# Performance work log

Hardware: AMD Instinct MI355X
Metric: run time of the kernel (lower is better)

## Reference

```python
import jax, jax.numpy as jnp
import numpy as np

POINT_SIZE = 1000000
LOC_DIM = 16
TIM_DIM = 16
POS_DIM = 32
INPUT_DIM = 5
HID = 32
EPS = 1e-5


def _linear(x, W, b):
    return x @ W.T + b


def _resnet(x, W1, b1, W2, b2):
    # Sequential(ReLU, Linear, ReLU, Linear, Dropout(eval=identity)); out = x + 0.3*net(x)
    h = jax.nn.relu(x)
    h = _linear(h, W1, b1)
    h = jax.nn.relu(h)
    h = _linear(h, W2, b2)
    return x + 0.3 * h


def _chain(x, rW1, rb1, rW2, rb2, W, b):
    for i in range(2):  # two ResNet blocks (fixed, structural)
        x = _resnet(x, rW1[i], rb1[i], rW2[i], rb2[i])
    return _linear(x, W, b)


def _mk_linear(key, out_dim, in_dim):
    k1, k2 = jax.random.split(key)
    s = 1.0 / np.sqrt(in_dim)
    W = jax.random.uniform(k1, (out_dim, in_dim), jnp.float32, -s, s)
    b = jax.random.uniform(k2, (out_dim,), jnp.float32, -s, s)
    return W, b


def _mk_res_stack(key, dim, n=2):
    ks = jax.random.split(key, 4 * n)
    W1s, b1s, W2s, b2s = [], [], [], []
    for i in range(n):
        W1, b1 = _mk_linear(ks[4 * i], dim, dim)
        W2, b2 = _mk_linear(ks[4 * i + 1], dim, dim)
        W1s.append(W1); b1s.append(b1); W2s.append(W2); b2s.append(b2)
    return jnp.stack(W1s), jnp.stack(b1s), jnp.stack(W2s), jnp.stack(b2s)


def setup_inputs() -> dict:
    key = jax.random.key(0)
    ks = iter(jax.random.split(key, 40))
    d = {}
    d["x"] = jax.random.randint(next(ks), (3,), 0, 24, dtype=jnp.int64 if jax.config.jax_enable_x64 else jnp.int32)
    d["hidden"] = jnp.zeros((1, 1, HID), jnp.float32)
    d["pos"] = 3
    # embeddings
    d["loc_emb"] = jax.random.normal(next(ks), (POINT_SIZE, LOC_DIM), jnp.float32)
    d["arr_emb"] = jax.random.normal(next(ks), (24, TIM_DIM), jnp.float32)
    d["dur_emb"] = jax.random.normal(next(ks), (24, TIM_DIM), jnp.float32)
    d["pos_emb"] = jax.random.normal(next(ks), (10, POS_DIM), jnp.float32)
    for name, dim in (("fc1", LOC_DIM), ("fc2", TIM_DIM), ("fc3", TIM_DIM)):
        rW1, rb1, rW2, rb2 = _mk_res_stack(next(ks), dim)
        W, b = _mk_linear(next(ks), INPUT_DIM, dim)
        d[f"{name}_rW1"], d[f"{name}_rb1"], d[f"{name}_rW2"], d[f"{name}_rb2"] = rW1, rb1, rW2, rb2
        d[f"{name}_W"], d[f"{name}_b"] = W, b
    # LayerNorm(15)
    d["ln_g"] = jnp.ones((3 * INPUT_DIM,), jnp.float32)
    d["ln_b"] = jnp.zeros((3 * INPUT_DIM,), jnp.float32)
    # ODE: Linear(5->32) + ResNet(32)
    d["ode_W"], d["ode_b"] = _mk_linear(next(ks), HID, INPUT_DIM)
    oW1, ob1, oW2, ob2 = _mk_res_stack(next(ks), HID, n=1)
    d["ode_rW1"], d["ode_rb1"], d["ode_rW2"], d["ode_rb2"] = oW1[0], ob1[0], oW2[0], ob2[0]
    # heads
    d["fc4_W"], d["fc4_b"] = _mk_linear(next(ks), POINT_SIZE, HID)
    d["fc5_W"], d["fc5_b"] = _mk_linear(next(ks), 24, HID)
    d["fc6_W"], d["fc6_b"] = _mk_linear(next(ks), 24, HID)
    # GRU (input 15, hidden 32)
    d["gru_Wih"], d["gru_bih"] = _mk_linear(next(ks), 3 * HID, 3 * INPUT_DIM)
    d["gru_Whh"], d["gru_bhh"] = _mk_linear(next(ks), 3 * HID, HID)
    return d


def reference(x, hidden, pos, loc_emb, arr_emb, dur_emb, pos_emb,
              fc1_rW1, fc1_rb1, fc1_rW2, fc1_rb2, fc1_W, fc1_b,
              fc2_rW1, fc2_rb1, fc2_rW2, fc2_rb2, fc2_W, fc2_b,
              fc3_rW1, fc3_rb1, fc3_rW2, fc3_rb2, fc3_W, fc3_b,
              ln_g, ln_b, ode_W, ode_b, ode_rW1, ode_rb1, ode_rW2, ode_rb2,
              fc4_W, fc4_b, fc5_W, fc5_b, fc6_W, fc6_b,
              gru_Wih, gru_bih, gru_Whh, gru_bhh):
    pos_e = pos_emb[pos]                                   # (32,)
    loc = _chain(loc_emb[x[0]], fc1_rW1, fc1_rb1, fc1_rW2, fc1_rb2, fc1_W, fc1_b)  # (5,)
    arr = _chain(arr_emb[x[1]], fc2_rW1, fc2_rb1, fc2_rW2, fc2_rb2, fc2_W, fc2_b)  # (5,)
    dur = _chain(dur_emb[x[2]], fc3_rW1, fc3_rb1, fc3_rW2, fc3_rb2, fc3_W, fc3_b)  # (5,)
    point = jnp.concatenate([loc, arr, dur])               # (15,)
    mu = jnp.mean(point)
    var = jnp.mean((point - mu) ** 2)
    point = (point - mu) * jax.lax.rsqrt(var + EPS) * ln_g + ln_b
    # hidden = hidden + ODE(dur)
    ode = _linear(dur, ode_W, ode_b)
    ode = _resnet(ode, ode_rW1, ode_rb1, ode_rW2, ode_rb2)
    h = hidden.reshape(-1) + ode                           # (32,)
    # single GRU step
    gi = gru_Wih @ point + gru_bih
    gh = gru_Whh @ h + gru_bhh
    i_r, i_z, i_n = jnp.split(gi, 3)
    h_r, h_z, h_n = jnp.split(gh, 3)
    r = jax.nn.sigmoid(i_r + h_r)
    z = jax.nn.sigmoid(i_z + h_z)
    n = jnp.tanh(i_n + r * h_n)
    h_new = (1.0 - z) * n + z * h                          # (32,) == out == new hidden
    next_loc = jax.nn.log_softmax(h_new @ fc4_W.T + fc4_b)
    next_arr = jax.nn.log_softmax((h_new + pos_e) @ fc5_W.T + fc5_b)
    next_dur = jax.nn.log_softmax(h_new @ fc6_W.T + fc6_b)
    return (next_loc, next_arr, next_dur, h_new.reshape(1, 1, HID))
```

## Files before the change

kernel.cpp:

```cpp
#include <hip/hip_runtime.h>
#include <math.h>

#define ROWS 1000000
#define K2_BLOCKS 1024
#define K2_THREADS 256

__global__ __launch_bounds__(128) void front_kernel(
    const int* __restrict__ x, const float* __restrict__ hidden, const int* __restrict__ pos,
    const float* __restrict__ loc_emb, const float* __restrict__ arr_emb,
    const float* __restrict__ dur_emb, const float* __restrict__ pos_emb,
    const float* __restrict__ f1rW1, const float* __restrict__ f1rb1,
    const float* __restrict__ f1rW2, const float* __restrict__ f1rb2,
    const float* __restrict__ f1W,   const float* __restrict__ f1b,
    const float* __restrict__ f2rW1, const float* __restrict__ f2rb1,
    const float* __restrict__ f2rW2, const float* __restrict__ f2rb2,
    const float* __restrict__ f2W,   const float* __restrict__ f2b,
    const float* __restrict__ f3rW1, const float* __restrict__ f3rb1,
    const float* __restrict__ f3rW2, const float* __restrict__ f3rb2,
    const float* __restrict__ f3W,   const float* __restrict__ f3b,
    const float* __restrict__ ln_g,  const float* __restrict__ ln_b,
    const float* __restrict__ ode_W, const float* __restrict__ ode_b,
    const float* __restrict__ oW1,   const float* __restrict__ ob1,
    const float* __restrict__ oW2,   const float* __restrict__ ob2,
    const float* __restrict__ fc5_W, const float* __restrict__ fc5_b,
    const float* __restrict__ fc6_W, const float* __restrict__ fc6_b,
    const float* __restrict__ gWih,  const float* __restrict__ gbih,
    const float* __restrict__ gWhh,  const float* __restrict__ gbhh,
    float* __restrict__ out, float* __restrict__ ws)
{
    __shared__ float e[3][16];
    __shared__ float tr[3][16];
    __shared__ float h1[3][16];
    __shared__ float praw[15];
    __shared__ float pnorm[15];
    __shared__ float ode0[32], odt[32], hvec[32], hnew[32], pe[32];
    __shared__ float gi[96], gh[96];
    __shared__ float a5[24], a6[24];
    __shared__ float red[4];

    const int t = threadIdx.x;

    if (t < 48) {
        int c = t >> 4, j = t & 15;
        const float* emb = (c == 0) ? (loc_emb + (size_t)x[0] * 16)
                         : (c == 1) ? (arr_emb + (size_t)x[1] * 16)
                                    : (dur_emb + (size_t)x[2] * 16);
        e[c][j] = emb[j];
    }
    if (t < 32) pe[t] = pos_emb[pos[0] * 32 + t];
    __syncthreads();

    for (int i = 0; i < 2; ++i) {
        if (t < 48) { int c = t >> 4, j = t & 15; tr[c][j] = fmaxf(e[c][j], 0.f); }
        __syncthreads();
        if (t < 48) {
            int c = t >> 4, j = t & 15;
            const float* W1 = ((c == 0) ? f1rW1 : (c == 1) ? f2rW1 : f3rW1) + i * 256 + j * 16;
            const float* b1 = ((c == 0) ? f1rb1 : (c == 1) ? f2rb1 : f3rb1) + i * 16;
            float a = b1[j];
            #pragma unroll
            for (int k = 0; k < 16; ++k) a += W1[k] * tr[c][k];
            h1[c][j] = fmaxf(a, 0.f);
        }
        __syncthreads();
        if (t < 48) {
            int c = t >> 4, j = t & 15;
            const float* W2 = ((c == 0) ? f1rW2 : (c == 1) ? f2rW2 : f3rW2) + i * 256 + j * 16;
            const float* b2 = ((c == 0) ? f1rb2 : (c == 1) ? f2rb2 : f3rb2) + i * 16;
            float a = b2[j];
            #pragma unroll
            for (int k = 0; k < 16; ++k) a += W2[k] * h1[c][k];
            e[c][j] += 0.3f * a;
        }
        __syncthreads();
    }

    if (t < 15) {
        int c = t / 5, q = t % 5;
        const float* W = ((c == 0) ? f1W : (c == 1) ? f2W : f3W) + q * 16;
        const float* b = ((c == 0) ? f1b : (c == 1) ? f2b : f3b);
        float a = b[q];
        #pragma unroll
        for (int k = 0; k < 16; ++k) a += W[k] * e[c][k];
        praw[t] = a;
    }
    __syncthreads();

    if (t == 0) {
        float mu = 0.f;
        for (int k = 0; k < 15; ++k) mu += praw[k];
        mu *= (1.f / 15.f);
        float var = 0.f;
        for (int k = 0; k < 15; ++k) { float d = praw[k] - mu; var += d * d; }
        var *= (1.f / 15.f);
        red[0] = mu;
        red[1] = rsqrtf(var + 1e-5f);
    }
    __syncthreads();
    if (t < 15) pnorm[t] = (praw[t] - red[0]) * red[1] * ln_g[t] + ln_b[t];

    if (t < 32) {
        float a = ode_b[t];
        const float* W = ode_W + t * 5;
        #pragma unroll
        for (int k = 0; k < 5; ++k) a += W[k] * praw[10 + k];
        ode0[t] = a;
    }
    __syncthreads();
    if (t < 32) {
        float a = ob1[t];
        const float* W = oW1 + t * 32;
        #pragma unroll
        for (int k = 0; k < 32; ++k) a += W[k] * fmaxf(ode0[k], 0.f);
        odt[t] = fmaxf(a, 0.f);
    }
    __syncthreads();
    if (t < 32) {
        float a = ob2[t];
        const float* W = oW2 + t * 32;
        #pragma unroll
        for (int k = 0; k < 32; ++k) a += W[k] * odt[k];
        hvec[t] = hidden[t] + ode0[t] + 0.3f * a;
    }
    __syncthreads();

    if (t < 96) {
        float a = gbih[t];
        const float* W = gWih + t * 15;
        #pragma unroll
        for (int k = 0; k < 15; ++k) a += W[k] * pnorm[k];
        gi[t] = a;
        float c2 = gbhh[t];
        const float* V = gWhh + t * 32;
        #pragma unroll
        for (int k = 0; k < 32; ++k) c2 += V[k] * hvec[k];
        gh[t] = c2;
    }
    __syncthreads();
    if (t < 32) {
        float r = 1.f / (1.f + expf(-(gi[t] + gh[t])));
        float z = 1.f / (1.f + expf(-(gi[32 + t] + gh[32 + t])));
        float n = tanhf(gi[64 + t] + r * gh[64 + t]);
        float hn = (1.f - z) * n + z * hvec[t];
        hnew[t] = hn;
        ws[t] = hn;
        out[ROWS + 48 + t] = hn;
    }
    __syncthreads();

    if (t < 24) {
        float a = fc5_b[t];
        const float* W = fc5_W + t * 32;
        #pragma unroll
        for (int k = 0; k < 32; ++k) a += W[k] * (hnew[k] + pe[k]);
        a5[t] = a;
        float b = fc6_b[t];
        const float* V = fc6_W + t * 32;
        #pragma unroll
        for (int k = 0; k < 32; ++k) b += V[k] * hnew[k];
        a6[t] = b;
    }
    __syncthreads();
    if (t == 0) {
        float m = -INFINITY;
        for (int k = 0; k < 24; ++k) m = fmaxf(m, a5[k]);
        float s = 0.f;
        for (int k = 0; k < 24; ++k) s += expf(a5[k] - m);
        red[2] = m + logf(s);
        m = -INFINITY;
        for (int k = 0; k < 24; ++k) m = fmaxf(m, a6[k]);
        s = 0.f;
        for (int k = 0; k < 24; ++k) s += expf(a6[k] - m);
        red[3] = m + logf(s);
    }
    __syncthreads();
    if (t < 24) {
        out[ROWS + t]      = a5[t] - red[2];
        out[ROWS + 24 + t] = a6[t] - red[3];
    }
}

__global__ __launch_bounds__(K2_THREADS) void logits_kernel(
    const float* __restrict__ W, const float* __restrict__ b,
    const float* __restrict__ ws_h, float* __restrict__ out,
    float* __restrict__ partials)
{
    __shared__ float hs[32];
    if (threadIdx.x < 32) hs[threadIdx.x] = ws_h[threadIdx.x];
    __syncthreads();

    float hr[32];
    #pragma unroll
    for (int k = 0; k < 32; ++k) hr[k] = hs[k];

    const float4* W4 = (const float4*)W;
    float m = -INFINITY, s = 0.f;

    for (int r = blockIdx.x * K2_THREADS + threadIdx.x; r < ROWS;
         r += K2_BLOCKS * K2_THREADS) {
        float acc = b[r];
        #pragma unroll
        for (int j = 0; j < 8; ++j) {
            float4 w = W4[(size_t)r * 8 + j];
            acc += w.x * hr[4 * j] + w.y * hr[4 * j + 1]
                 + w.z * hr[4 * j + 2] + w.w * hr[4 * j + 3];
        }
        out[r] = acc;
        if (acc > m) { s = s * expf(m - acc) + 1.f; m = acc; }
        else         { s += expf(acc - m); }
    }

    __shared__ float sm[K2_THREADS], ss[K2_THREADS];
    sm[threadIdx.x] = m; ss[threadIdx.x] = s;
    __syncthreads();
    for (int off = K2_THREADS / 2; off > 0; off >>= 1) {
        if (threadIdx.x < off) {
            float m2 = sm[threadIdx.x + off], s2 = ss[threadIdx.x + off];
            float M  = fmaxf(sm[threadIdx.x], m2);
            ss[threadIdx.x] = ss[threadIdx.x] * expf(sm[threadIdx.x] - M)
                            + s2 * expf(m2 - M);
            sm[threadIdx.x] = M;
        }
        __syncthreads();
    }
    if (threadIdx.x == 0) {
        partials[2 * blockIdx.x]     = sm[0];
        partials[2 * blockIdx.x + 1] = ss[0];
    }
}

__global__ __launch_bounds__(256) void lse_reduce_kernel(
    const float* __restrict__ partials, float* __restrict__ lse)
{
    __shared__ float sm[256], ss[256];
    const int t = threadIdx.x;
    float m = -INFINITY, s = 0.f;
    for (int i = t; i < K2_BLOCKS; i += 256) {
        float m2 = partials[2 * i], s2 = partials[2 * i + 1];
        float M = fmaxf(m, m2);
        s = s * ((m == -INFINITY) ? 0.f : expf(m - M)) + s2 * expf(m2 - M);
        m = M;
    }
    sm[t] = m; ss[t] = s;
    __syncthreads();
    for (int off = 128; off > 0; off >>= 1) {
        if (t < off) {
            float m2 = sm[t + off], s2 = ss[t + off];
            float M = fmaxf(sm[t], m2);
            ss[t] = ss[t] * expf(sm[t] - M) + s2 * expf(m2 - M);
            sm[t] = M;
        }
        __syncthreads();
    }
    if (t == 0) lse[0] = sm[0] + logf(ss[0]);
}

__global__ __launch_bounds__(256) void finalize_kernel(
    float* __restrict__ out, const float* __restrict__ lse)
{
    const int r4 = blockIdx.x * 256 + threadIdx.x;
    if (r4 < ROWS / 4) {
        const float l = lse[0];
        float4* o4 = (float4*)out;
        float4 v = o4[r4];
        v.x -= l; v.y -= l; v.z -= l; v.w -= l;
        o4[r4] = v;
    }
}

extern "C" void kernel_launch(void* const* d_in, const int* in_sizes, int n_in,
                              void* d_out, int out_size, void* d_ws, size_t ws_size,
                              hipStream_t stream) {
    const int*   x       = (const int*)  d_in[0];
    const float* hidden  = (const float*)d_in[1];
    const int*   pos     = (const int*)  d_in[2];
    const float* loc_emb = (const float*)d_in[3];
    const float* arr_emb = (const float*)d_in[4];
    const float* dur_emb = (const float*)d_in[5];
    const float* pos_emb = (const float*)d_in[6];
    const float* f1rW1 = (const float*)d_in[7];
    const float* f1rb1 = (const float*)d_in[8];
    const float* f1rW2 = (const float*)d_in[9];
    const float* f1rb2 = (const float*)d_in[10];
    const float* f1W   = (const float*)d_in[11];
    const float* f1b   = (const float*)d_in[12];
    const float* f2rW1 = (const float*)d_in[13];
    const float* f2rb1 = (const float*)d_in[14];
    const float* f2rW2 = (const float*)d_in[15];
    const float* f2rb2 = (const float*)d_in[16];
    const float* f2W   = (const float*)d_in[17];
    const float* f2b   = (const float*)d_in[18];
    const float* f3rW1 = (const float*)d_in[19];
    const float* f3rb1 = (const float*)d_in[20];
    const float* f3rW2 = (const float*)d_in[21];
    const float* f3rb2 = (const float*)d_in[22];
    const float* f3W   = (const float*)d_in[23];
    const float* f3b   = (const float*)d_in[24];
    const float* ln_g  = (const float*)d_in[25];
    const float* ln_b  = (const float*)d_in[26];
    const float* ode_W = (const float*)d_in[27];
    const float* ode_b = (const float*)d_in[28];
    const float* oW1   = (const float*)d_in[29];
    const float* ob1   = (const float*)d_in[30];
    const float* oW2   = (const float*)d_in[31];
    const float* ob2   = (const float*)d_in[32];
    const float* fc4_W = (const float*)d_in[33];
    const float* fc4_b = (const float*)d_in[34];
    const float* fc5_W = (const float*)d_in[35];
    const float* fc5_b = (const float*)d_in[36];
    const float* fc6_W = (const float*)d_in[37];
    const float* fc6_b = (const float*)d_in[38];
    const float* gWih  = (const float*)d_in[39];
    const float* gbih  = (const float*)d_in[40];
    const float* gWhh  = (const float*)d_in[41];
    const float* gbhh  = (const float*)d_in[42];

    float* out = (float*)d_out;
    float* wsf = (float*)d_ws;
    float* ws_h        = wsf;
    float* ws_lse      = wsf + 32;
    float* ws_partials = wsf + 64;

    front_kernel<<<1, 128, 0, stream>>>(
        x, hidden, pos, loc_emb, arr_emb, dur_emb, pos_emb,
        f1rW1, f1rb1, f1rW2, f1rb2, f1W, f1b,
        f2rW1, f2rb1, f2rW2, f2rb2, f2W, f2b,
        f3rW1, f3rb1, f3rW2, f3rb2, f3W, f3b,
        ln_g, ln_b, ode_W, ode_b, oW1, ob1, oW2, ob2,
        fc5_W, fc5_b, fc6_W, fc6_b, gWih, gbih, gWhh, gbhh,
        out, ws_h);

    logits_kernel<<<K2_BLOCKS, K2_THREADS, 0, stream>>>(
        fc4_W, fc4_b, ws_h, out, ws_partials);

    lse_reduce_kernel<<<1, 256, 0, stream>>>(ws_partials, ws_lse);

    finalize_kernel<<<(ROWS / 4 + 255) / 256, 256, 0, stream>>>(out, ws_lse);
}
```

Before: 47.19 us.

## Fuse front MLP, logits and LSE into one kernel with redundant per-block prologue

Folds the single-block front kernel into the logits kernel: every block recomputes the small GRU/MLP front end itself, so the front-to-logits launch and handoff disappear. The separate LSE-reduce kernel is merged into finalize, with each block re-reducing the partials. Going from four launches to two is meant to remove launch and serialization gaps. The logits loop is restructured so each wave handles 8 rows per step with coalesced float4 loads and a shuffle reduction. Idle waves prefetch small weights and the first fc4 tiles to warm the cache. Because all 8 lanes of a row group add the same logit, the sum is corrected by subtracting ln 8. The cost is redundant front work in every block and extra prefetch traffic.

Measured after the change: 73.49 us. 1.56x slower.

```diff
diff --git a/kernel.cpp b/kernel.cpp
--- a/kernel.cpp
+++ b/kernel.cpp
@@ -2,52 +2,83 @@
 #include <math.h>
 
 #define ROWS 1000000
-#define K2_BLOCKS 1024
-#define K2_THREADS 256
-
-__global__ __launch_bounds__(128) void front_kernel(
-    const int* __restrict__ x, const float* __restrict__ hidden, const int* __restrict__ pos,
-    const float* __restrict__ loc_emb, const float* __restrict__ arr_emb,
-    const float* __restrict__ dur_emb, const float* __restrict__ pos_emb,
-    const float* __restrict__ f1rW1, const float* __restrict__ f1rb1,
-    const float* __restrict__ f1rW2, const float* __restrict__ f1rb2,
-    const float* __restrict__ f1W,   const float* __restrict__ f1b,
-    const float* __restrict__ f2rW1, const float* __restrict__ f2rb1,
-    const float* __restrict__ f2rW2, const float* __restrict__ f2rb2,
-    const float* __restrict__ f2W,   const float* __restrict__ f2b,
-    const float* __restrict__ f3rW1, const float* __restrict__ f3rb1,
-    const float* __restrict__ f3rW2, const float* __restrict__ f3rb2,
-    const float* __restrict__ f3W,   const float* __restrict__ f3b,
-    const float* __restrict__ ln_g,  const float* __restrict__ ln_b,
-    const float* __restrict__ ode_W, const float* __restrict__ ode_b,
-    const float* __restrict__ oW1,   const float* __restrict__ ob1,
-    const float* __restrict__ oW2,   const float* __restrict__ ob2,
-    const float* __restrict__ fc5_W, const float* __restrict__ fc5_b,
-    const float* __restrict__ fc6_W, const float* __restrict__ fc6_b,
-    const float* __restrict__ gWih,  const float* __restrict__ gbih,
-    const float* __restrict__ gWhh,  const float* __restrict__ gbhh,
-    float* __restrict__ out, float* __restrict__ ws)
+#define NBLK 1024
+#define NTHR 256
+#define WAVES (NTHR / 64)
+#define GW (NBLK * WAVES)
+#define ITER ((ROWS + GW * 8 - 1) / (GW * 8))
+#define NBLK_B 977
+#define LN8 2.0794415416798357f
+
+struct Params {
+    const int*   x; const float* hidden; const int* pos;
+    const float* loc_emb; const float* arr_emb; const float* dur_emb; const float* pos_emb;
+    const float* f1rW1; const float* f1rb1; const float* f1rW2; const float* f1rb2;
+    const float* f1W;   const float* f1b;
+    const float* f2rW1; const float* f2rb1; const float* f2rW2; const float* f2rb2;
+    const float* f2W;   const float* f2b;
+    const float* f3rW1; const float* f3rb1; const float* f3rW2; const float* f3rb2;
+    const float* f3W;   const float* f3b;
+    const float* ln_g;  const float* ln_b;
+    const float* ode_W; const float* ode_b;
+    const float* oW1;   const float* ob1; const float* oW2; const float* ob2;
+    const float* fc4_W; const float* fc4_b;
+    const float* fc5_W; const float* fc5_b;
+    const float* fc6_W; const float* fc6_b;
+    const float* gWih;  const float* gbih; const float* gWhh; const float* gbhh;
+    float* out; float* ws;
+};
+
+__device__ __forceinline__ float warmA(const float* ptr, int n4, int wt) {
+    float a = 0.f;
+    const float4* v = (const float4*)ptr;
+    for (int i = wt; i < n4; i += 192) { float4 w = v[i]; a += w.x + w.y + w.z + w.w; }
+    return a;
+}
+
+__global__ __launch_bounds__(NTHR) void bigkernel(Params p)
 {
-    __shared__ float e[3][16];
-    __shared__ float tr[3][16];
-    __shared__ float h1[3][16];
-    __shared__ float praw[15];
-    __shared__ float pnorm[15];
+    const int t   = threadIdx.x;
+    const int bid = blockIdx.x;
+    const int l   = t & 63;
+    const int wid = t >> 6;
+    const int wg  = bid * WAVES + wid;
+    const float4* W4 = (const float4*)p.fc4_W;
+
+    if (t >= 64) {
+        const int wt = t - 64;
+        float a0 = warmA(p.gWhh, 768, wt);
+        a0 += warmA(p.gWih, 360, wt);
+        a0 += warmA(p.oW1, 256, wt)   + warmA(p.oW2, 256, wt);
+        a0 += warmA(p.fc5_W, 192, wt) + warmA(p.fc6_W, 192, wt);
+        a0 += warmA(p.f1rW1, 128, wt) + warmA(p.f1rW2, 128, wt);
+        a0 += warmA(p.f2rW1, 128, wt) + warmA(p.f2rW2, 128, wt);
+        a0 += warmA(p.f3rW1, 128, wt) + warmA(p.f3rW2, 128, wt);
+        a0 += warmA(p.ode_W, 40, wt);
+        a0 += warmA(p.f1W, 20, wt) + warmA(p.f2W, 20, wt) + warmA(p.f3W, 20, wt);
+        #pragma unroll
+        for (int c = 0; c < 4; ++c) {
+            float4 w = W4[(size_t)(c * GW + wg) * 64 + l];
+            a0 += w.x + w.y + w.z + w.w;
+        }
+        asm volatile("" :: "v"(a0));
+    }
+
+    __shared__ float e[3][16], tr[3][16], h1[3][16];
+    __shared__ float praw[15], pnorm[15];
     __shared__ float ode0[32], odt[32], hvec[32], hnew[32], pe[32];
     __shared__ float gi[96], gh[96];
     __shared__ float a5[24], a6[24];
     __shared__ float red[4];
 
-    const int t = threadIdx.x;
-
     if (t < 48) {
         int c = t >> 4, j = t & 15;
-        const float* emb = (c == 0) ? (loc_emb + (size_t)x[0] * 16)
-                         : (c == 1) ? (arr_emb + (size_t)x[1] * 16)
-                                    : (dur_emb + (size_t)x[2] * 16);
+        const float* emb = (c == 0) ? (p.loc_emb + (size_t)p.x[0] * 16)
+                         : (c == 1) ? (p.arr_emb + (size_t)p.x[1] * 16)
+                                    : (p.dur_emb + (size_t)p.x[2] * 16);
         e[c][j] = emb[j];
     }
-    if (t < 32) pe[t] = pos_emb[pos[0] * 32 + t];
+    if (t < 32) pe[t] = p.pos_emb[p.pos[0] * 32 + t];
     __syncthreads();
 
     for (int i = 0; i < 2; ++i) {
@@ -55,8 +86,8 @@
         __syncthreads();
         if (t < 48) {
             int c = t >> 4, j = t & 15;
-            const float* W1 = ((c == 0) ? f1rW1 : (c == 1) ? f2rW1 : f3rW1) + i * 256 + j * 16;
-            const float* b1 = ((c == 0) ? f1rb1 : (c == 1) ? f2rb1 : f3rb1) + i * 16;
+            const float* W1 = ((c == 0) ? p.f1rW1 : (c == 1) ? p.f2rW1 : p.f3rW1) + i * 256 + j * 16;
+            const float* b1 = ((c == 0) ? p.f1rb1 : (c == 1) ? p.f2rb1 : p.f3rb1) + i * 16;
             float a = b1[j];
             #pragma unroll
             for (int k = 0; k < 16; ++k) a += W1[k] * tr[c][k];
@@ -65,8 +96,8 @@
         __syncthreads();
         if (t < 48) {
             int c = t >> 4, j = t & 15;
-            const float* W2 = ((c == 0) ? f1rW2 : (c == 1) ? f2rW2 : f3rW2) + i * 256 + j * 16;
-            const float* b2 = ((c == 0) ? f1rb2 : (c == 1) ? f2rb2 : f3rb2) + i * 16;
+            const float* W2 = ((c == 0) ? p.f1rW2 : (c == 1) ? p.f2rW2 : p.f3rW2) + i * 256 + j * 16;
+            const float* b2 = ((c == 0) ? p.f1rb2 : (c == 1) ? p.f2rb2 : p.f3rb2) + i * 16;
             float a = b2[j];
             #pragma unroll
             for (int k = 0; k < 16; ++k) a += W2[k] * h1[c][k];
@@ -77,8 +108,8 @@
 
     if (t < 15) {
         int c = t / 5, q = t % 5;
-        const float* W = ((c == 0) ? f1W : (c == 1) ? f2W : f3W) + q * 16;
-        const float* b = ((c == 0) ? f1b : (c == 1) ? f2b : f3b);
+        const float* W = ((c == 0) ? p.f1W : (c == 1) ? p.f2W : p.f3W) + q * 16;
+        const float* b = ((c == 0) ? p.f1b : (c == 1) ? p.f2b : p.f3b);
         float a = b[q];
         #pragma unroll
         for (int k = 0; k < 16; ++k) a += W[k] * e[c][k];
@@ -97,44 +128,44 @@
         red[1] = rsqrtf(var + 1e-5f);
     }
     __syncthreads();
-    if (t < 15) pnorm[t] = (praw[t] - red[0]) * red[1] * ln_g[t] + ln_b[t];
-
+    if (t < 15) pnorm[t] = (praw[t] - red[0]) * red[1] * p.ln_g[t] + p.ln_b[t];
     if (t < 32) {
-        float a = ode_b[t];
-        const float* W = ode_W + t * 5;
+        float a = p.ode_b[t];
+        const float* W = p.ode_W + t * 5;
         #pragma unroll
         for (int k = 0; k < 5; ++k) a += W[k] * praw[10 + k];
         ode0[t] = a;
     }
     __syncthreads();
     if (t < 32) {
-        float a = ob1[t];
-        const float* W = oW1 + t * 32;
+        float a = p.ob1[t];
+        const float* W = p.oW1 + t * 32;
         #pragma unroll
         for (int k = 0; k < 32; ++k) a += W[k] * fmaxf(ode0[k], 0.f);
         odt[t] = fmaxf(a, 0.f);
     }
     __syncthreads();
     if (t < 32) {
-        float a = ob2[t];
-        const float* W = oW2 + t * 32;
+        float a = p.ob2[t];
+        const float* W = p.oW2 + t * 32;
         #pragma unroll
         for (int k = 0; k < 32; ++k) a += W[k] * odt[k];
-        hvec[t] = hidden[t] + ode0[t] + 0.3f * a;
-    }
-    __syncthreads();
-
-    if (t < 96) {
-        float a = gbih[t];
-        const float* W = gWih + t * 15;
-        #pragma unroll
-        for (int k = 0; k < 15; ++k) a += W[k] * pnorm[k];
-        gi[t] = a;
-        float c2 = gbhh[t];
-        const float* V = gWhh + t * 32;
-        #pragma unroll
-        for (int k = 0; k < 32; ++k) c2 += V[k] * hvec[k];
-        gh[t] = c2;
+        hvec[t] = p.hidden[t] + ode0[t] + 0.3f * a;
+    }
+    __syncthreads();
+    if (t < 64) {
+        for (int q = t; q < 96; q += 64) {
+            float a = p.gbih[q];
+            const float* W = p.gWih + q * 15;
+            #pragma unroll
+            for (int k = 0; k < 15; ++k) a += W[k] * pnorm[k];
+            gi[q] = a;
+            float c2 = p.gbhh[q];
+            const float* V = p.gWhh + q * 32;
+            #pragma unroll
+            for (int k = 0; k < 32; ++k) c2 += V[k] * hvec[k];
+            gh[q] = c2;
+        }
     }
     __syncthreads();
     if (t < 32) {
@@ -143,19 +174,17 @@
         float n = tanhf(gi[64 + t] + r * gh[64 + t]);
         float hn = (1.f - z) * n + z * hvec[t];
         hnew[t] = hn;
-        ws[t] = hn;
-        out[ROWS + 48 + t] = hn;
-    }
-    __syncthreads();
-
+        if (bid == 0) p.out[ROWS + 48 + t] = hn;
+    }
+    __syncthreads();
     if (t < 24) {
-        float a = fc5_b[t];
-        const float* W = fc5_W + t * 32;
+        float a = p.fc5_b[t];
+        const float* W = p.fc5_W + t * 32;
         #pragma unroll
         for (int k = 0; k < 32; ++k) a += W[k] * (hnew[k] + pe[k]);
         a5[t] = a;
-        float b = fc6_b[t];
-        const float* V = fc6_W + t * 32;
+        float b = p.fc6_b[t];
+        const float* V = p.fc6_W + t * 32;
         #pragma unroll
         for (int k = 0; k < 32; ++k) b += V[k] * hnew[k];
         a6[t] = b;
@@ -174,166 +203,139 @@
         red[3] = m + logf(s);
     }
     __syncthreads();
-    if (t < 24) {
-        out[ROWS + t]      = a5[t] - red[2];
-        out[ROWS + 24 + t] = a6[t] - red[3];
-    }
-}
-
-__global__ __launch_bounds__(K2_THREADS) void logits_kernel(
-    const float* __restrict__ W, const float* __restrict__ b,
-    const float* __restrict__ ws_h, float* __restrict__ out,
-    float* __restrict__ partials)
-{
-    __shared__ float hs[32];
-    if (threadIdx.x < 32) hs[threadIdx.x] = ws_h[threadIdx.x];
-    __syncthreads();
+    if (bid == 0 && t < 24) {
+        p.out[ROWS + t]      = a5[t] - red[2];
+        p.out[ROWS + 24 + t] = a6[t] - red[3];
+    }
 
     float hr[32];
     #pragma unroll
-    for (int k = 0; k < 32; ++k) hr[k] = hs[k];
-
-    const float4* W4 = (const float4*)W;
+    for (int k = 0; k < 32; ++k) hr[k] = hnew[k];
+
+    const int j = l & 7;
+    const int g = l >> 3;
     float m = -INFINITY, s = 0.f;
 
-    for (int r = blockIdx.x * K2_THREADS + threadIdx.x; r < ROWS;
-         r += K2_BLOCKS * K2_THREADS) {
-        float acc = b[r];
-        #pragma unroll
-        for (int j = 0; j < 8; ++j) {
-            float4 w = W4[(size_t)r * 8 + j];
-            acc += w.x * hr[4 * j] + w.y * hr[4 * j + 1]
-                 + w.z * hr[4 * j + 2] + w.w * hr[4 * j + 3];
-        }
-        out[r] = acc;
-        if (acc > m) { s = s * expf(m - acc) + 1.f; m = acc; }
-        else         { s += expf(acc - m); }
-    }
-
-    __shared__ float sm[K2_THREADS], ss[K2_THREADS];
-    sm[threadIdx.x] = m; ss[threadIdx.x] = s;
-    __syncthreads();
-    for (int off = K2_THREADS / 2; off > 0; off >>= 1) {
-        if (threadIdx.x < off) {
-            float m2 = sm[threadIdx.x + off], s2 = ss[threadIdx.x + off];
-            float M  = fmaxf(sm[threadIdx.x], m2);
-            ss[threadIdx.x] = ss[threadIdx.x] * expf(sm[threadIdx.x] - M)
-                            + s2 * expf(m2 - M);
-            sm[threadIdx.x] = M;
-        }
-        __syncthreads();
-    }
-    if (threadIdx.x == 0) {
-        partials[2 * blockIdx.x]     = sm[0];
-        partials[2 * blockIdx.x + 1] = ss[0];
-    }
+    for (int c = 0; c < ITER; ++c) {
+        const int rb = (c * GW + wg) * 8;
+        const int my_row = rb + g;
+        if (my_row < ROWS) {
+            float4 w = W4[(size_t)rb * 8 + l];
+            float pp = w.x * hr[4*j] + w.y * hr[4*j+1]
+                     + w.z * hr[4*j+2] + w.w * hr[4*j+3];
+            pp += __shfl_xor(pp, 1);
+            pp += __shfl_xor(pp, 2);
+            pp += __shfl_xor(pp, 4);
+            float logit = pp + p.fc4_b[my_row];
+            if (j == 0) p.out[my_row] = logit;
+            if (logit > m) { s = s * __expf(m - logit) + 1.f; m = logit; }
+            else           { s += __expf(logit - m); }
+        }
+    }
+
+    __shared__ float sm[NTHR], ss[NTHR];
+    sm[t] = m; ss[t] = s;
+    __syncthreads();
+    for (int off = NTHR / 2; off > 0; off >>= 1) {
+        if (t < off) {
+            float m2 = sm[t + off], s2 = ss[t + off];
+            float M  = fmaxf(sm[t], m2);
+            ss[t] = ss[t] * expf(sm[t] - M) + s2 * expf(m2 - M);
+            sm[t] = M;
+        }
+        __syncthreads();
+    }
+    if (t == 0) { p.ws[2 * bid] = sm[0]; p.ws[2 * bid + 1] = ss[0]; }
 }
 
-__global__ __launch_bounds__(256) void lse_reduce_kernel(
-    const float* __restrict__ partials, float* __restrict__ lse)
+__global__ __launch_bounds__(256) void finalize_kernel(
+    const float* __restrict__ partials, float* __restrict__ out)
 {
     __shared__ float sm[256], ss[256];
+    __shared__ float lse_sh;
     const int t = threadIdx.x;
-    float m = -INFINITY, s = 0.f;
-    for (int i = t; i < K2_BLOCKS; i += 256) {
+
+    float fm = -INFINITY, fs = 0.f;
+    for (int i = t; i < NBLK; i += 256) {
         float m2 = partials[2 * i], s2 = partials[2 * i + 1];
-        float M = fmaxf(m, m2);
-        s = s * ((m == -INFINITY) ? 0.f : expf(m - M)) + s2 * expf(m2 - M);
-        m = M;
-    }
-    sm[t] = m; ss[t] = s;
+        float M  = fmaxf(fm, m2);
+        fs = fs * expf(fm - M) + s2 * expf(m2 - M);
+        fm = M;
+    }
+    sm[t] = fm; ss[t] = fs;
     __syncthreads();
     for (int off = 128; off > 0; off >>= 1) {
         if (t < off) {
             float m2 = sm[t + off], s2 = ss[t + off];
-            float M = fmaxf(sm[t], m2);
+            float M  = fmaxf(sm[t], m2);
             ss[t] = ss[t] * expf(sm[t] - M) + s2 * expf(m2 - M);
             sm[t] = M;
         }
         __syncthreads();
     }
-    if (t == 0) lse[0] = sm[0] + logf(ss[0]);
-}
-
-__global__ __launch_bounds__(256) void finalize_kernel(
-    float* __restrict__ out, const float* __restrict__ lse)
-{
-    const int r4 = blockIdx.x * 256 + threadIdx.x;
-    if (r4 < ROWS / 4) {
-        const float l = lse[0];
+    if (t == 0) lse_sh = sm[0] + logf(ss[0]) - LN8;
+    __syncthreads();
+    const float lse = lse_sh;
+
+    const int idx = blockIdx.x * 256 + t;
+    if (idx < ROWS / 4) {
         float4* o4 = (float4*)out;
-        float4 v = o4[r4];
-        v.x -= l; v.y -= l; v.z -= l; v.w -= l;
-        o4[r4] = v;
+        float4 v = o4[idx];
+        v.x -= lse; v.y -= lse; v.z -= lse; v.w -= lse;
+        o4[idx] = v;
     }
 }
 
 extern "C" void kernel_launch(void* const* d_in, const int* in_sizes, int n_in,
                               void* d_out, int out_size, void* d_ws, size_t ws_size,
                               hipStream_t stream) {
-    const int*   x       = (const int*)  d_in[0];
-    const float* hidden  = (const float*)d_in[1];
-    const int*   pos     = (const int*)  d_in[2];
-    const float* loc_emb = (const float*)d_in[3];
-    const float* arr_emb = (const float*)d_in[4];
-    const float* dur_emb = (const float*)d_in[5];
-    const float* pos_emb = (const float*)d_in[6];
-    const float* f1rW1 = (const float*)d_in[7];
-    const float* f1rb1 = (const float*)d_in[8];
-    const float* f1rW2 = (const float*)d_in[9];
-    const float* f1rb2 = (const float*)d_in[10];
-    const float* f1W   = (const float*)d_in[11];
-    const float* f1b   = (const float*)d_in[12];
-    const float* f2rW1 = (const float*)d_in[13];
-    const float* f2rb1 = (const float*)d_in[14];
-    const float* f2rW2 = (const float*)d_in[15];
-    const float* f2rb2 = (const float*)d_in[16];
-    const float* f2W   = (const float*)d_in[17];
-    const float* f2b   = (const float*)d_in[18];
-    const float* f3rW1 = (const float*)d_in[19];
-    const float* f3rb1 = (const float*)d_in[20];
-    const float* f3rW2 = (const float*)d_in[21];
-    const float* f3rb2 = (const float*)d_in[22];
-    const float* f3W   = (const float*)d_in[23];
-    const float* f3b   = (const float*)d_in[24];
-    const float* ln_g  = (const float*)d_in[25];
-    const float* ln_b  = (const float*)d_in[26];
-    const float* ode_W = (const float*)d_in[27];
-    const float* ode_b = (const float*)d_in[28];
-    const float* oW1   = (const float*)d_in[29];
-    const float* ob1   = (const float*)d_in[30];
-    const float* oW2   = (const float*)d_in[31];
-    const float* ob2   = (const float*)d_in[32];
-    const float* fc4_W = (const float*)d_in[33];
-    const float* fc4_b = (const float*)d_in[34];
-    const float* fc5_W = (const float*)d_in[35];
-    const float* fc5_b = (const float*)d_in[36];
-    const float* fc6_W = (const float*)d_in[37];
-    const float* fc6_b = (const float*)d_in[38];
-    const float* gWih  = (const float*)d_in[39];
-    const float* gbih  = (const float*)d_in[40];
-    const float* gWhh  = (const float*)d_in[41];
-    const float* gbhh  = (const float*)d_in[42];
-
-    float* out = (float*)d_out;
-    float* wsf = (float*)d_ws;
-    float* ws_h        = wsf;
-    float* ws_lse      = wsf + 32;
-    float* ws_partials = wsf + 64;
-
-    front_kernel<<<1, 128, 0, stream>>>(
-        x, hidden, pos, loc_emb, arr_emb, dur_emb, pos_emb,
-        f1rW1, f1rb1, f1rW2, f1rb2, f1W, f1b,
-        f2rW1, f2rb1, f2rW2, f2rb2, f2W, f2b,
-        f3rW1, f3rb1, f3rW2, f3rb2, f3W, f3b,
-        ln_g, ln_b, ode_W, ode_b, oW1, ob1, oW2, ob2,
-        fc5_W, fc5_b, fc6_W, fc6_b, gWih, gbih, gWhh, gbhh,
-        out, ws_h);
-
-    logits_kernel<<<K2_BLOCKS, K2_THREADS, 0, stream>>>(
-        fc4_W, fc4_b, ws_h, out, ws_partials);
-
-    lse_reduce_kernel<<<1, 256, 0, stream>>>(ws_partials, ws_lse);
-
-    finalize_kernel<<<(ROWS / 4 + 255) / 256, 256, 0, stream>>>(out, ws_lse);
+    Params pr;
+    pr.x       = (const int*)  d_in[0];
+    pr.hidden  = (const float*)d_in[1];
+    pr.pos     = (const int*)  d_in[2];
+    pr.loc_emb = (const float*)d_in[3];
+    pr.arr_emb = (const float*)d_in[4];
+    pr.dur_emb = (const float*)d_in[5];
+    pr.pos_emb = (const float*)d_in[6];
+    pr.f1rW1 = (const float*)d_in[7];
+    pr.f1rb1 = (const float*)d_in[8];
+    pr.f1rW2 = (const float*)d_in[9];
+    pr.f1rb2 = (const float*)d_in[10];
+    pr.f1W   = (const float*)d_in[11];
+    pr.f1b   = (const float*)d_in[12];
+    pr.f2rW1 = (const float*)d_in[13];
+    pr.f2rb1 = (const float*)d_in[14];
+    pr.f2rW2 = (const float*)d_in[15];
+    pr.f2rb2 = (const float*)d_in[16];
+    pr.f2W   = (const float*)d_in[17];
+    pr.f2b   = (const float*)d_in[18];
+    pr.f3rW1 = (const float*)d_in[19];
+    pr.f3rb1 = (const float*)d_in[20];
+    pr.f3rW2 = (const float*)d_in[21];
+    pr.f3rb2 = (const float*)d_in[22];
+    pr.f3W   = (const float*)d_in[23];
+    pr.f3b   = (const float*)d_in[24];
+    pr.ln_g  = (const float*)d_in[25];
+    pr.ln_b  = (const float*)d_in[26];
+    pr.ode_W = (const float*)d_in[27];
+    pr.ode_b = (const float*)d_in[28];
+    pr.oW1   = (const float*)d_in[29];
+    pr.ob1   = (const float*)d_in[30];
+    pr.oW2   = (const float*)d_in[31];
+    pr.ob2   = (const float*)d_in[32];
+    pr.fc4_W = (const float*)d_in[33];
+    pr.fc4_b = (const float*)d_in[34];
+    pr.fc5_W = (const float*)d_in[35];
+    pr.fc5_b = (const float*)d_in[36];
+    pr.fc6_W = (const float*)d_in[37];
+    pr.fc6_b = (const float*)d_in[38];
+    pr.gWih  = (const float*)d_in[39];
+    pr.gbih  = (const float*)d_in[40];
+    pr.gWhh  = (const float*)d_in[41];
+    pr.gbhh  = (const float*)d_in[42];
+    pr.out = (float*)d_out;
+    pr.ws  = (float*)d_ws;
+
+    bigkernel<<<NBLK, NTHR, 0, stream>>>(pr);
+    finalize_kernel<<<NBLK_B, 256, 0, stream>>>((const float*)d_ws, (float*)d_out);
 }
```

## Fuse LSE reduction into finalize and use one-row-per-thread logits grid

Applied to the files above, without the earlier changes.

The grid-stride logits kernel with 1024 blocks becomes a one-row-per-thread grid of 3907 blocks, which drops the per-row online-softmax exp in each thread. The single-block LSE reduce kernel is removed. Every finalize block now redundantly reduces the 3907 partials itself before subtracting the log-sum-exp, saving one kernel launch at the cost of repeated partial reads and exps in each block. Fast __expf replaces expf in the reductions.

New measurement: 45.15 us. -4.3%, faster.

```diff
diff --git a/kernel.cpp b/kernel.cpp
--- a/kernel.cpp
+++ b/kernel.cpp
@@ -1,9 +1,12 @@
 #include <hip/hip_runtime.h>
 #include <math.h>
+#include <float.h>
 
 #define ROWS 1000000
-#define K2_BLOCKS 1024
-#define K2_THREADS 256
+#define NTHR 256
+#define NBLK_L 3907
+#define NBLK_B 977
+#define NEG_BIG (-3.0e38f)
 
 __global__ __launch_bounds__(128) void front_kernel(
     const int* __restrict__ x, const float* __restrict__ hidden, const int* __restrict__ pos,
@@ -28,11 +31,8 @@
     const float* __restrict__ gWhh,  const float* __restrict__ gbhh,
     float* __restrict__ out, float* __restrict__ ws)
 {
-    __shared__ float e[3][16];
-    __shared__ float tr[3][16];
-    __shared__ float h1[3][16];
-    __shared__ float praw[15];
-    __shared__ float pnorm[15];
+    __shared__ float e[3][16], tr[3][16], h1[3][16];
+    __shared__ float praw[15], pnorm[15];
     __shared__ float ode0[32], odt[32], hvec[32], hnew[32], pe[32];
     __shared__ float gi[96], gh[96];
     __shared__ float a5[24], a6[24];
@@ -98,7 +98,6 @@
     }
     __syncthreads();
     if (t < 15) pnorm[t] = (praw[t] - red[0]) * red[1] * ln_g[t] + ln_b[t];
-
     if (t < 32) {
         float a = ode_b[t];
         const float* W = ode_W + t * 5;
@@ -123,7 +122,6 @@
         hvec[t] = hidden[t] + ode0[t] + 0.3f * a;
     }
     __syncthreads();
-
     if (t < 96) {
         float a = gbih[t];
         const float* W = gWih + t * 15;
@@ -147,7 +145,6 @@
         out[ROWS + 48 + t] = hn;
     }
     __syncthreads();
-
     if (t < 24) {
         float a = fc5_b[t];
         const float* W = fc5_W + t * 32;
@@ -180,91 +177,83 @@
     }
 }
 
-__global__ __launch_bounds__(K2_THREADS) void logits_kernel(
+__global__ __launch_bounds__(NTHR) void logits_kernel(
     const float* __restrict__ W, const float* __restrict__ b,
     const float* __restrict__ ws_h, float* __restrict__ out,
-    float* __restrict__ partials)
+    float2* __restrict__ partials)
 {
     __shared__ float hs[32];
     if (threadIdx.x < 32) hs[threadIdx.x] = ws_h[threadIdx.x];
     __syncthreads();
 
-    float hr[32];
-    #pragma unroll
-    for (int k = 0; k < 32; ++k) hr[k] = hs[k];
-
-    const float4* W4 = (const float4*)W;
-    float m = -INFINITY, s = 0.f;
-
-    for (int r = blockIdx.x * K2_THREADS + threadIdx.x; r < ROWS;
-         r += K2_BLOCKS * K2_THREADS) {
+    const int t = threadIdx.x;
+    const int r = blockIdx.x * NTHR + t;
+
+    float m = NEG_BIG, s = 0.f;
+    if (r < ROWS) {
+        const float4* W4 = (const float4*)W;
+        float4 w[8];
+        #pragma unroll
+        for (int j = 0; j < 8; ++j) w[j] = W4[(size_t)r * 8 + j];
         float acc = b[r];
         #pragma unroll
-        for (int j = 0; j < 8; ++j) {
-            float4 w = W4[(size_t)r * 8 + j];
-            acc += w.x * hr[4 * j] + w.y * hr[4 * j + 1]
-                 + w.z * hr[4 * j + 2] + w.w * hr[4 * j + 3];
+        for (int j = 0; j < 8; ++j)
+            acc += w[j].x * hs[4*j] + w[j].y * hs[4*j+1]
+                 + w[j].z * hs[4*j+2] + w[j].w * hs[4*j+3];
+        out[r] = acc;
+        m = acc; s = 1.f;
+    }
+
+    __shared__ float sm[NTHR], ss[NTHR];
+    sm[t] = m; ss[t] = s;
+    __syncthreads();
+    for (int off = NTHR / 2; off > 0; off >>= 1) {
+        if (t < off) {
+            float m2 = sm[t + off], s2 = ss[t + off];
+            float M  = fmaxf(sm[t], m2);
+            ss[t] = ss[t] * __expf(sm[t] - M) + s2 * __expf(m2 - M);
+            sm[t] = M;
         }
-        out[r] = acc;
-        if (acc > m) { s = s * expf(m - acc) + 1.f; m = acc; }
-        else         { s += expf(acc - m); }
-    }
-
-    __shared__ float sm[K2_THREADS], ss[K2_THREADS];
-    sm[threadIdx.x] = m; ss[threadIdx.x] = s;
-    __syncthreads();
-    for (int off = K2_THREADS / 2; off > 0; off >>= 1) {
-        if (threadIdx.x < off) {
-            float m2 = sm[threadIdx.x + off], s2 = ss[threadIdx.x + off];
-            float M  = fmaxf(sm[threadIdx.x], m2);
-            ss[threadIdx.x] = ss[threadIdx.x] * expf(sm[threadIdx.x] - M)
-                            + s2 * expf(m2 - M);
-            sm[threadIdx.x] = M;
-        }
-        __syncthreads();
-    }
-    if (threadIdx.x == 0) {
-        partials[2 * blockIdx.x]     = sm[0];
-        partials[2 * blockIdx.x + 1] = ss[0];
-    }
+        __syncthreads();
+    }
+    if (t == 0) partials[blockIdx.x] = make_float2(sm[0], ss[0]);
 }
 
-__global__ __launch_bounds__(256) void lse_reduce_kernel(
-    const float* __restrict__ partials, float* __restrict__ lse)
+__global__ __launch_bounds__(256) void finalize_kernel(
+    const float2* __restrict__ partials, float* __restrict__ out)
 {
     __shared__ float sm[256], ss[256];
+    __shared__ float lse_sh;
     const int t = threadIdx.x;
-    float m = -INFINITY, s = 0.f;
-    for (int i = t; i < K2_BLOCKS; i += 256) {
-        float m2 = partials[2 * i], s2 = partials[2 * i + 1];
-        float M = fmaxf(m, m2);
-        s = s * ((m == -INFINITY) ? 0.f : expf(m - M)) + s2 * expf(m2 - M);
-        m = M;
-    }
-    sm[t] = m; ss[t] = s;
+
+    float fm = NEG_BIG, fs = 0.f;
+    for (int i = t; i < NBLK_L; i += 256) {
+        float2 p2 = partials[i];
+        float M = fmaxf(fm, p2.x);
+        fs = fs * __expf(fm - M) + p2.y * __expf(p2.x - M);
+        fm = M;
+    }
+    sm[t] = fm; ss[t] = fs;
     __syncthreads();
     for (int off = 128; off > 0; off >>= 1) {
         if (t < off) {
             float m2 = sm[t + off], s2 = ss[t + off];
-            float M = fmaxf(sm[t], m2);
-            ss[t] = ss[t] * expf(sm[t] - M) + s2 * expf(m2 - M);
+            float M  = fmaxf(sm[t], m2);
+            ss[t] = ss[t] * __expf(sm[t] - M) + s2 * __expf(m2 - M);
             sm[t] = M;
         }
         __syncthreads();
     }
-    if (t == 0) lse[0] = sm[0] + logf(ss[0]);
-}
-
-__global__ __launch_bounds__(256) void finalize_kernel(
-    float* __restrict__ out, const float* __restrict__ lse)
-{
-    const int r4 = blockIdx.x * 256 + threadIdx.x;
-    if (r4 < ROWS / 4) {
-        const float l = lse[0];
+    if (t == 0) lse_sh = sm[0] + logf(ss[0]);
+    __syncthreads();
+    const float lse = lse_sh;
+
+    const int idx = blockIdx.x * 256 + t;
+    if (idx < ROWS / 4) {
         float4* o4 = (float4*)out;
-        float4 v = o4[r4];
-        v.x -= l; v.y -= l; v.z -= l; v.w -= l;
-        o4[r4] = v;
+        float4 v = o4[idx];
+        v.x -= lse; v.y -= lse; v.z -= lse; v.w -= lse;
+        o4[idx] = v;
     }
 }
 
@@ -317,9 +306,8 @@
 
     float* out = (float*)d_out;
     float* wsf = (float*)d_ws;
-    float* ws_h        = wsf;
-    float* ws_lse      = wsf + 32;
-    float* ws_partials = wsf + 64;
+    float*  ws_h        = wsf;
+    float2* ws_partials = (float2*)(wsf + 64);
 
     front_kernel<<<1, 128, 0, stream>>>(
         x, hidden, pos, loc_emb, arr_emb, dur_emb, pos_emb,
@@ -330,10 +318,8 @@
         fc5_W, fc5_b, fc6_W, fc6_b, gWih, gbih, gWhh, gbhh,
         out, ws_h);
 
-    logits_kernel<<<K2_BLOCKS, K2_THREADS, 0, stream>>>(
+    logits_kernel<<<NBLK_L, NTHR, 0, stream>>>(
         fc4_W, fc4_b, ws_h, out, ws_partials);
 
-    lse_reduce_kernel<<<1, 256, 0, stream>>>(ws_partials, ws_lse);
-
-    finalize_kernel<<<(ROWS / 4 + 255) / 256, 256, 0, stream>>>(out, ws_lse);
+    finalize_kernel<<<NBLK_B, 256, 0, stream>>>(ws_partials, out);
 }
```
